# Kernel tuning notes

Measured on AMD Instinct MI355X. Metric: run time of the kernel, lower is better.

## Reference

```python
import jax, jax.numpy as jnp
import numpy as np

HIST_LEN = 100  # STDP history cap in the original module


def setup_inputs() -> dict:
    key = jax.random.key(0)
    ks = jax.random.split(key, 5)
    H, B = 1024, 16384
    return {
        "x": jax.random.normal(ks[0], (B, H), dtype=jnp.float32),
        "weights": jax.random.normal(ks[1], (H, H), dtype=jnp.float32) * 0.1,
        "meta_plasticity": jnp.ones((H,), dtype=jnp.float32),
        "pre_hist": jax.random.normal(ks[2], (HIST_LEN, H), dtype=jnp.float32) * 0.1,
        "post_hist": jax.random.normal(ks[3], (HIST_LEN, H), dtype=jnp.float32) * 0.1,
        "activity_history": jnp.zeros((1000,), dtype=jnp.float32),
        "history_pointer": 5,
        "stdp_window": jnp.float32(20.0),
        "stdp_decay": jnp.float32(0.1),
        "target_activity": jnp.float32(0.1),
        "homeostatic_rate": jnp.float32(0.01),
        "meta_learning_rate": jnp.float32(0.001),
    }


def reference(x, weights, meta_plasticity, pre_hist, post_hist,
              activity_history, history_pointer, stdp_window, stdp_decay,
              target_activity, homeostatic_rate, meta_learning_rate):
    # --- forward matmul: weights * meta_plasticity scales columns (broadcast over rows)
    output = x @ (weights * meta_plasticity)  # [B, H]

    # --- STDP update (vectorized form of the python loop over the history) ---
    # append current mean activities, pop oldest (steady-state length == HIST_LEN)
    pre = jnp.concatenate([pre_hist[1:], x.mean(axis=0)[None]], axis=0)       # [L, H]
    post = jnp.concatenate([post_hist[1:], output.mean(axis=0)[None]], axis=0)
    L = HIST_LEN
    i = jnp.arange(L, dtype=jnp.float32)
    dt = (L - i) * stdp_window
    w = 0.01 * jnp.exp(-dt * stdp_decay)                                      # [L]
    pos_w = jnp.where(i < L - 1, w, 0.0)   # i < len-1 branch
    neg_w = jnp.where(i > 0, w, 0.0)       # i > 0 branch
    # sum_i pos_w[i] * outer(post[-1], pre[i]) = outer(post[-1], pos_w @ pre)
    dW = jnp.outer(post[-1], pos_w @ pre) - jnp.outer(neg_w @ post, pre[-1])
    new_w = jnp.clip(weights + dW, -1.0, 1.0)

    # --- homeostatic plasticity ---
    hist = activity_history.at[history_pointer].set(output.mean())
    activity_diff = target_activity - hist.mean()
    new_w = jnp.clip(new_w * (1.0 + homeostatic_rate * activity_diff), -1.0, 1.0)

    # --- meta plasticity ---
    new_meta = jnp.clip(
        meta_plasticity + meta_learning_rate * (output.mean(axis=0) - meta_plasticity),
        0.0, 2.0)

    return output, new_w, new_meta, hist
```

## Files before the change

kernel.cpp:

```cpp
#include <hip/hip_runtime.h>
#include <hip/hip_bf16.h>

#define H 1024
#define BATCH 16384

typedef unsigned short u16;
typedef u16 u16x8 __attribute__((ext_vector_type(8)));
typedef __bf16 bf16x8 __attribute__((ext_vector_type(8)));
typedef float f32x4 __attribute__((ext_vector_type(4)));

typedef __attribute__((address_space(3))) unsigned int lds_uint;
typedef __attribute__((address_space(1))) const unsigned int glob_uint;

__device__ __forceinline__ u16 f2bf(float f) {
  unsigned int u = __float_as_uint(f);
  u += 0x7fffu + ((u >> 16) & 1u);
  return (u16)(u >> 16);
}

#define WS_XSUMP   0
#define WS_XSUM    (WS_XSUMP + 256 * H)
#define WS_ORAWP   (WS_XSUM + H)
#define WS_POSVP   (WS_ORAWP + 16 * H)
#define WS_NEGHP   (WS_POSVP + 5 * H)
#define WS_SCRATCH (WS_NEGHP + 5 * H)
#define WS_BF16    (WS_SCRATCH + 16)

__global__ __launch_bounds__(256) void prep_kernel(const float* __restrict__ X,
                                                   const float* __restrict__ W,
                                                   u16* __restrict__ Xb,
                                                   u16* __restrict__ Wbt,
                                                   float* __restrict__ ws,
                                                   const float* __restrict__ pre,
                                                   const float* __restrict__ post,
                                                   const float* __restrict__ win,
                                                   const float* __restrict__ dec) {
  __shared__ __align__(16) u16 t[64][72];
  const int b = blockIdx.x, tid = threadIdx.x;
  if (b < 256) {
    size_t r0 = (size_t)b * 64;
    float s0 = 0.f, s1 = 0.f, s2 = 0.f, s3 = 0.f;
#pragma unroll 4
    for (int r = 0; r < 64; ++r) {
      size_t off = (r0 + r) * H + tid * 4;
      const float4 v = *(const float4*)&X[off];
      ushort4 h;
      h.x = f2bf(v.x); h.y = f2bf(v.y); h.z = f2bf(v.z); h.w = f2bf(v.w);
      *(ushort4*)&Xb[off] = h;
      s0 += v.x; s1 += v.y; s2 += v.z; s3 += v.w;
    }
    float* row = &ws[WS_XSUMP + b * H];
    row[tid * 4 + 0] = s0; row[tid * 4 + 1] = s1;
    row[tid * 4 + 2] = s2; row[tid * 4 + 3] = s3;
  } else if (b < 512) {
    const int b2 = b - 256;
    const int n0 = (b2 & 15) * 64, k0 = (b2 >> 4) * 64;
    const int rb = tid >> 4, c4 = tid & 15;
#pragma unroll
    for (int i = 0; i < 4; ++i) {
      int r = rb + i * 16;
      const float4 v = *(const float4*)&W[(size_t)(k0 + r) * H + n0 + c4 * 4];
      t[c4 * 4 + 0][r] = f2bf(v.x);
      t[c4 * 4 + 1][r] = f2bf(v.y);
      t[c4 * 4 + 2][r] = f2bf(v.z);
      t[c4 * 4 + 3][r] = f2bf(v.w);
    }
    __syncthreads();
    const int seg = tid & 7;
#pragma unroll
    for (int p = 0; p < 2; ++p) {
      int wr = p * 32 + (tid >> 3);
      *(u16x8*)&Wbt[(size_t)(n0 + wr) * H + k0 + seg * 8] = *(const u16x8*)&t[wr][seg * 8];
    }
  } else {
    const int b2 = b - 512;
    const int col = (b2 & 3) * 256 + tid;
    const int seg = b2 >> 2;
    const int t0 = 1 + seg * 20;
    int tend = t0 + 20; if (tend > 100) tend = 100;
    float wd = win[0] * dec[0];
    float ps = 0.f, ns = 0.f;
    for (int tt = t0; tt < tend; ++tt) {
      float w = 0.01f * expf(-(float)(101 - tt) * wd);
      ps += w * pre[tt * H + col];
      if (tt >= 2) ns += w * post[tt * H + col];
    }
    ws[WS_POSVP + seg * H + col] = ps;
    ws[WS_NEGHP + seg * H + col] = ns;
  }
}

__global__ __launch_bounds__(512, 2) void gemm_vm_kernel(const u16* __restrict__ Xb,
                                                         const u16* __restrict__ Wbt,
                                                         const float* __restrict__ meta,
                                                         const float* __restrict__ W,
                                                         float* __restrict__ ws,
                                                         float* __restrict__ out) {
  __shared__ __align__(16) u16 lds[65536];

  const int b = blockIdx.x, tid = threadIdx.x;

  if (b >= 256) {
    float* xs = (float*)lds;
    const int b2 = b - 256;
    const int jx = b2 & 3, ky = b2 >> 2;
    if (tid < 64) {
      float s = 0.f;
      const float* p = &ws[WS_XSUMP + ky * 64 + tid];
#pragma unroll 8
      for (int q = 0; q < 256; ++q) s += p[q * H];
      xs[tid] = s;
      if (jx == 0) ws[WS_XSUM + ky * 64 + tid] = s;
    }
    __syncthreads();
    if (tid < 256) {
      const int j = jx * 256 + tid;
      float s = 0.f;
#pragma unroll 8
      for (int k = 0; k < 64; ++k) s += xs[k] * W[(size_t)(ky * 64 + k) * H + j];
      ws[WS_ORAWP + ky * H + j] = s * (1.0f / (float)BATCH);
    }
    return;
  }

  const int tile = ((b & 7) << 5) | (b >> 3);
  const int mt = tile >> 2, nt = tile & 3;
  const size_t row0 = (size_t)mt * 256;
  const int col0 = nt * 256;
  const int wid = tid >> 6, lane = tid & 63;
  const int wm = wid >> 2, wn = wid & 3;
  const int quad = lane >> 4, l16 = lane & 15;
  const int xsw = l16 & 7;

  const int srow = lane >> 3;
  const int schunk = (lane & 7) ^ (srow & 7);

  auto stageA = [&](int t, int h) {
#pragma unroll
    for (int s = 0; s < 2; ++s) {
      const u16* ga = &Xb[(row0 + h * 128 + s * 64 + wid * 8 + srow) * H + t * 64 + schunk * 8];
      lds_uint* ld = (lds_uint*)&lds[(((2 * t + h) & 3) * 8192) + s * 4096 + wid * 512];
      __builtin_amdgcn_global_load_lds((glob_uint*)ga, ld, 16, 0, 0);
    }
  };
  auto stageB = [&](int t, int h) {
#pragma unroll
    for (int s = 0; s < 2; ++s) {
      const u16* gb = &Wbt[(size_t)(col0 + h * 128 + s * 64 + wid * 8 + srow) * H + t * 64 + schunk * 8];
      lds_uint* ld = (lds_uint*)&lds[32768 + (((2 * t + h) & 3) * 8192) + s * 4096 + wid * 512];
      __builtin_amdgcn_global_load_lds((glob_uint*)gb, ld, 16, 0, 0);
    }
  };

  f32x4 acc[8][4];
#pragma unroll
  for (int i = 0; i < 8; ++i)
#pragma unroll
    for (int j = 0; j < 4; ++j) acc[i][j] = (f32x4){0.f, 0.f, 0.f, 0.f};

  stageA(0, 0); stageA(0, 1); stageB(0, 0); stageB(0, 1); stageB(1, 0); stageB(1, 1);
  asm volatile("s_waitcnt vmcnt(2)" ::: "memory");
  __builtin_amdgcn_s_barrier();

  for (int t = 0; t < 16; ++t) {
    const int aslot = ((2 * t + wm) & 3) * 8192;
    const int bslot = 32768 + ((2 * t + (wn >> 1)) & 3) * 8192;
    const int brl = (wn & 1) * 64;
    bf16x8 bv[4][2];

    if (t < 15) { stageA(t + 1, 0); stageA(t + 1, 1); }
#pragma unroll
    for (int fn = 0; fn < 4; ++fn)
#pragma unroll
      for (int ks = 0; ks < 2; ++ks)
        bv[fn][ks] = __builtin_bit_cast(bf16x8,
          *(const u16x8*)&lds[bslot + (brl + fn * 16 + l16) * 64 + (((ks * 4 + quad) ^ xsw) * 8)]);
    {
      bf16x8 av[4][2];
#pragma unroll
      for (int fi = 0; fi < 4; ++fi)
#pragma unroll
        for (int ks = 0; ks < 2; ++ks)
          av[fi][ks] = __builtin_bit_cast(bf16x8,
            *(const u16x8*)&lds[aslot + (fi * 16 + l16) * 64 + (((ks * 4 + quad) ^ xsw) * 8)]);
      asm volatile("s_waitcnt lgkmcnt(0)" ::: "memory");
      __builtin_amdgcn_sched_barrier(0);
      __builtin_amdgcn_s_setprio(1);
#pragma unroll
      for (int fi = 0; fi < 4; ++fi)
#pragma unroll
        for (int fn = 0; fn < 4; ++fn)
#pragma unroll
          for (int ks = 0; ks < 2; ++ks)
            acc[fi][fn] = __builtin_amdgcn_mfma_f32_16x16x32_bf16(
                av[fi][ks], bv[fn][ks], acc[fi][fn], 0, 0, 0);
      __builtin_amdgcn_s_setprio(0);
    }
    __builtin_amdgcn_s_barrier();

    if (t < 14) { stageB(t + 2, 0); stageB(t + 2, 1); }
    {
      bf16x8 av[4][2];
#pragma unroll
      for (int fi = 0; fi < 4; ++fi)
#pragma unroll
        for (int ks = 0; ks < 2; ++ks)
          av[fi][ks] = __builtin_bit_cast(bf16x8,
            *(const u16x8*)&lds[aslot + ((4 + fi) * 16 + l16) * 64 + (((ks * 4 + quad) ^ xsw) * 8)]);
      asm volatile("s_waitcnt lgkmcnt(0)" ::: "memory");
      __builtin_amdgcn_sched_barrier(0);
      __builtin_amdgcn_s_setprio(1);
#pragma unroll
      for (int fi = 0; fi < 4; ++fi)
#pragma unroll
        for (int fn = 0; fn < 4; ++fn)
#pragma unroll
          for (int ks = 0; ks < 2; ++ks)
            acc[4 + fi][fn] = __builtin_amdgcn_mfma_f32_16x16x32_bf16(
                av[fi][ks], bv[fn][ks], acc[4 + fi][fn], 0, 0, 0);
      __builtin_amdgcn_s_setprio(0);
    }
    if (t < 14)       asm volatile("s_waitcnt vmcnt(2)" ::: "memory");
    else if (t == 14) asm volatile("s_waitcnt vmcnt(0)" ::: "memory");
    __builtin_amdgcn_s_barrier();
  }

  float mcol[4];
#pragma unroll
  for (int fn = 0; fn < 4; ++fn) mcol[fn] = meta[col0 + wn * 64 + fn * 16 + l16];
#pragma unroll
  for (int fm = 0; fm < 8; ++fm) {
#pragma unroll
    for (int fn = 0; fn < 4; ++fn) {
      const int col = col0 + wn * 64 + fn * 16 + l16;
#pragma unroll
      for (int r = 0; r < 4; ++r) {
        size_t row = row0 + wm * 128 + fm * 16 + quad * 4 + r;
        out[row * H + col] = acc[fm][fn][r] * mcol[fn];
      }
    }
  }
}

__global__ __launch_bounds__(256) void tail_kernel(const float* __restrict__ W,
                                                   const float* __restrict__ meta,
                                                   const float* __restrict__ act,
                                                   const int* __restrict__ ptr,
                                                   const float* __restrict__ targ,
                                                   const float* __restrict__ homeo,
                                                   const float* __restrict__ mlr,
                                                   const float* __restrict__ win,
                                                   const float* __restrict__ dec,
                                                   const float* __restrict__ ws,
                                                   float* __restrict__ out_w,
                                                   float* __restrict__ meta_out,
                                                   float* __restrict__ hist_out) {
  __shared__ float r1[4], r2[4];
  const int r = blockIdx.x;
  const int t = threadIdx.x;
  const int c4 = t * 4;

  f32x4 oraw = (f32x4){0.f, 0.f, 0.f, 0.f};
#pragma unroll
  for (int i = 0; i < 16; ++i) {
    const float4 v = *(const float4*)&ws[WS_ORAWP + i * H + c4];
    oraw[0] += v.x; oraw[1] += v.y; oraw[2] += v.z; oraw[3] += v.w;
  }
  const float4 mv = *(const float4*)&meta[c4];
  f32x4 om;
  om[0] = mv.x * oraw[0]; om[1] = mv.y * oraw[1];
  om[2] = mv.z * oraw[2]; om[3] = mv.w * oraw[3];

  float s1 = om[0] + om[1] + om[2] + om[3];
  float s2 = 0.f;
#pragma unroll
  for (int j = 0; j < 4; ++j) {
    int idx = t + j * 256;
    if (idx < 1000) s2 += act[idx];
  }
#pragma unroll
  for (int o = 32; o > 0; o >>= 1) {
    s1 += __shfl_down(s1, o, 64);
    s2 += __shfl_down(s2, o, 64);
  }
  if ((t & 63) == 0) { r1[t >> 6] = s1; r2[t >> 6] = s2; }
  __syncthreads();
  const float ts1 = r1[0] + r1[1] + r1[2] + r1[3];
  const float ts2 = r2[0] + r2[1] + r2[2] + r2[3];
  const float total_mean = ts1 / (float)H;
  const int p = ptr[0];
  const float hist_mean = (ts2 - act[p] + total_mean) / 1000.f;
  const float scale = 1.f + homeo[0] * (targ[0] - hist_mean);
  const float w99 = 0.01f * expf(-win[0] * dec[0]);

  float oraw_r = 0.f;
#pragma unroll
  for (int i = 0; i < 16; ++i) oraw_r += ws[WS_ORAWP + i * H + r];
  const float om_r = meta[r] * oraw_r;
  float negh_r = 0.f;
#pragma unroll
  for (int i = 0; i < 5; ++i) negh_r += ws[WS_NEGHP + i * H + r];
  const float neg_r = negh_r + w99 * om_r;

  f32x4 pv = (f32x4){0.f, 0.f, 0.f, 0.f};
#pragma unroll
  for (int i = 0; i < 5; ++i) {
    const float4 v = *(const float4*)&ws[WS_POSVP + i * H + c4];
    pv[0] += v.x; pv[1] += v.y; pv[2] += v.z; pv[3] += v.w;
  }
  const float4 xv = *(const float4*)&ws[WS_XSUM + c4];
  float xx[4] = {xv.x, xv.y, xv.z, xv.w};
  const float4 wv = *(const float4*)&W[(size_t)r * H + c4];
  float wx[4] = {wv.x, wv.y, wv.z, wv.w};
  float4 o;
  float ox[4];
#pragma unroll
  for (int i = 0; i < 4; ++i) {
    float v = wx[i] + om_r * pv[i] - neg_r * (xx[i] * (1.0f / (float)BATCH));
    v = fminf(fmaxf(v, -1.f), 1.f);
    v = v * scale;
    ox[i] = fminf(fmaxf(v, -1.f), 1.f);
  }
  o.x = ox[0]; o.y = ox[1]; o.z = ox[2]; o.w = ox[3];
  *(float4*)&out_w[(size_t)r * H + c4] = o;

  if (r == 0) {
    float4 nm;
    float nx[4] = {mv.x, mv.y, mv.z, mv.w};
    float nr[4];
#pragma unroll
    for (int i = 0; i < 4; ++i) {
      float v = nx[i] + mlr[0] * (om[i] - nx[i]);
      nr[i] = fminf(fmaxf(v, 0.f), 2.f);
    }
    nm.x = nr[0]; nm.y = nr[1]; nm.z = nr[2]; nm.w = nr[3];
    *(float4*)&meta_out[c4] = nm;
#pragma unroll
    for (int j = 0; j < 4; ++j) {
      int idx = t + j * 256;
      if (idx < 1000) hist_out[idx] = (idx == p) ? total_mean : act[idx];
    }
  }
}

__global__ __launch_bounds__(256) void colsum_kernel(const float* __restrict__ x,
                                                     float* __restrict__ xsum) {
  int col = blockIdx.x * 256 + threadIdx.x;
  size_t r0 = (size_t)blockIdx.y * 256;
  float s = 0.f;
#pragma unroll 8
  for (int r = 0; r < 256; ++r) s += x[(r0 + r) * H + col];
  atomicAdd(&xsum[col], s);
}

__global__ __launch_bounds__(256) void gemm_fallback_kernel(const float* __restrict__ X,
                                                            const float* __restrict__ W,
                                                            const float* __restrict__ meta,
                                                            float* __restrict__ out) {
  __shared__ __align__(16) u16 lA[128][40];
  __shared__ __align__(16) u16 lB[128][40];
  const int tid = threadIdx.x;
  const int wave = tid >> 6;
  const int lane = tid & 63;
  const int quad = lane >> 4;
  const int l16 = lane & 15;
  const int wm = wave >> 1, wn = wave & 1;
  const size_t row0 = (size_t)blockIdx.x * 128;
  const int col0 = blockIdx.y * 128;
  f32x4 acc[4][4];
#pragma unroll
  for (int i = 0; i < 4; ++i)
#pragma unroll
    for (int j = 0; j < 4; ++j) acc[i][j] = (f32x4){0.f, 0.f, 0.f, 0.f};
  for (int k0 = 0; k0 < H; k0 += 32) {
#pragma unroll
    for (int i = 0; i < 4; ++i) {
      int idx = i * 256 + tid;
      int r = idx >> 3, c4 = idx & 7;
      const float4 v = *(const float4*)&X[(row0 + r) * H + k0 + c4 * 4];
      ushort4 h;
      h.x = f2bf(v.x); h.y = f2bf(v.y); h.z = f2bf(v.z); h.w = f2bf(v.w);
      *(ushort4*)&lA[r][c4 * 4] = h;
    }
#pragma unroll
    for (int i = 0; i < 4; ++i) {
      int idx = i * 256 + tid;
      int kk = idx >> 5, c4 = idx & 31;
      const float4 v = *(const float4*)&W[(size_t)(k0 + kk) * H + col0 + c4 * 4];
      lB[c4 * 4 + 0][kk] = f2bf(v.x);
      lB[c4 * 4 + 1][kk] = f2bf(v.y);
      lB[c4 * 4 + 2][kk] = f2bf(v.z);
      lB[c4 * 4 + 3][kk] = f2bf(v.w);
    }
    __syncthreads();
    bf16x8 av[4], bv[4];
#pragma unroll
    for (int f = 0; f < 4; ++f) {
      av[f] = __builtin_bit_cast(bf16x8, *(const u16x8*)&lA[wm * 64 + f * 16 + l16][quad * 8]);
      bv[f] = __builtin_bit_cast(bf16x8, *(const u16x8*)&lB[wn * 64 + f * 16 + l16][quad * 8]);
    }
#pragma unroll
    for (int fm = 0; fm < 4; ++fm)
#pragma unroll
      for (int fn = 0; fn < 4; ++fn)
        acc[fm][fn] = __builtin_amdgcn_mfma_f32_16x16x32_bf16(av[fm], bv[fn], acc[fm][fn], 0, 0, 0);
    __syncthreads();
  }
  float mcol[4];
#pragma unroll
  for (int fn = 0; fn < 4; ++fn) mcol[fn] = meta[col0 + wn * 64 + fn * 16 + l16];
#pragma unroll
  for (int fm = 0; fm < 4; ++fm) {
#pragma unroll
    for (int fn = 0; fn < 4; ++fn) {
      int col = col0 + wn * 64 + fn * 16 + l16;
#pragma unroll
      for (int r = 0; r < 4; ++r) {
        size_t row = row0 + wm * 64 + fm * 16 + quad * 4 + r;
        out[row * H + col] = acc[fm][fn][r] * mcol[fn];
      }
    }
  }
}

__global__ __launch_bounds__(256) void vecmat_kernel(const float* __restrict__ W,
                                                     const float* __restrict__ xsum,
                                                     float* __restrict__ outraw) {
  int j = blockIdx.x * 256 + threadIdx.x;
  int k0 = blockIdx.y * 64;
  float s = 0.f;
#pragma unroll 8
  for (int k = 0; k < 64; ++k) s += xsum[k0 + k] * W[(size_t)(k0 + k) * H + j];
  atomicAdd(&outraw[j], s * (1.0f / (float)BATCH));
}

__global__ __launch_bounds__(256) void stdpvec_kernel(const float* __restrict__ pre,
                                                      const float* __restrict__ post,
                                                      const float* __restrict__ win,
                                                      const float* __restrict__ dec,
                                                      float* __restrict__ posv,
                                                      float* __restrict__ negh) {
  int col = blockIdx.x * 256 + threadIdx.x;
  int t0 = 1 + blockIdx.y * 20;
  float wd = win[0] * dec[0];
  float ps = 0.f, ns = 0.f;
  int tend = t0 + 20;
  if (tend > 100) tend = 100;
  for (int t = t0; t < tend; ++t) {
    float w = 0.01f * expf(-(float)(101 - t) * wd);
    ps += w * pre[t * H + col];
    if (t >= 2) ns += w * post[t * H + col];
  }
  atomicAdd(&posv[col], ps);
  atomicAdd(&negh[col], ns);
}

__global__ __launch_bounds__(1024) void finalize_kernel(const float* __restrict__ meta,
                                                        const float* __restrict__ act,
                                                        const int* __restrict__ ptr,
                                                        const float* __restrict__ targ,
                                                        const float* __restrict__ homeo,
                                                        const float* __restrict__ mlr,
                                                        const float* __restrict__ outraw,
                                                        float* __restrict__ outmean,
                                                        float* __restrict__ scalep,
                                                        float* __restrict__ meta_out,
                                                        float* __restrict__ hist_out) {
  __shared__ float r1[16], r2[16];
  __shared__ float sc[2];
  int t = threadIdx.x;
  float om = meta[t] * outraw[t];
  outmean[t] = om;
  float a = (t < 1000) ? act[t] : 0.f;
  float s1 = om, s2 = a;
#pragma unroll
  for (int o = 32; o > 0; o >>= 1) {
    s1 += __shfl_down(s1, o, 64);
    s2 += __shfl_down(s2, o, 64);
  }
  if ((t & 63) == 0) { r1[t >> 6] = s1; r2[t >> 6] = s2; }
  __syncthreads();
  if (t == 0) {
    float ts1 = 0.f, ts2 = 0.f;
#pragma unroll
    for (int i = 0; i < 16; ++i) { ts1 += r1[i]; ts2 += r2[i]; }
    float total_mean = ts1 / (float)H;
    int p = ptr[0];
    float hist_mean = (ts2 - act[p] + total_mean) / 1000.f;
    float diff = targ[0] - hist_mean;
    sc[0] = 1.f + homeo[0] * diff;
    sc[1] = total_mean;
    scalep[0] = sc[0];
  }
  __syncthreads();
  float nm = meta[t] + mlr[0] * (om - meta[t]);
  nm = fminf(fmaxf(nm, 0.f), 2.f);
  meta_out[t] = nm;
  if (t < 1000) hist_out[t] = (t == ptr[0]) ? sc[1] : act[t];
}

__global__ __launch_bounds__(256) void neww_kernel(const float* __restrict__ W,
                                                   const float* __restrict__ outmean,
                                                   const float* __restrict__ posv,
                                                   const float* __restrict__ negh,
                                                   const float* __restrict__ xsum,
                                                   const float* __restrict__ scalep,
                                                   const float* __restrict__ win,
                                                   const float* __restrict__ dec,
                                                   float* __restrict__ out) {
  int idx4 = blockIdx.x * 256 + threadIdx.x;
  int rr = idx4 >> 8;
  int c4 = (idx4 & 255) * 4;
  float w99 = 0.01f * expf(-win[0] * dec[0]);
  float scale = scalep[0];
  float om_r = outmean[rr];
  float neg_r = negh[rr] + w99 * om_r;
  const float4 wv = *(const float4*)&W[(size_t)rr * H + c4];
  const float4 pv = *(const float4*)&posv[c4];
  const float4 xv = *(const float4*)&xsum[c4];
  float4 o;
  float vx[4] = {wv.x, wv.y, wv.z, wv.w};
  float px[4] = {pv.x, pv.y, pv.z, pv.w};
  float xx[4] = {xv.x, xv.y, xv.z, xv.w};
  float ox[4];
#pragma unroll
  for (int i = 0; i < 4; ++i) {
    float v = vx[i] + om_r * px[i] - neg_r * (xx[i] * (1.0f / (float)BATCH));
    v = fminf(fmaxf(v, -1.f), 1.f);
    v = v * scale;
    ox[i] = fminf(fmaxf(v, -1.f), 1.f);
  }
  o.x = ox[0]; o.y = ox[1]; o.z = ox[2]; o.w = ox[3];
  *(float4*)&out[(size_t)rr * H + c4] = o;
}

extern "C" void kernel_launch(void* const* d_in, const int* in_sizes, int n_in,
                              void* d_out, int out_size, void* d_ws, size_t ws_size,
                              hipStream_t stream) {
  const float* x     = (const float*)d_in[0];
  const float* W     = (const float*)d_in[1];
  const float* meta  = (const float*)d_in[2];
  const float* pre   = (const float*)d_in[3];
  const float* post  = (const float*)d_in[4];
  const float* act   = (const float*)d_in[5];
  const int*   ptr   = (const int*)d_in[6];
  const float* win   = (const float*)d_in[7];
  const float* dec   = (const float*)d_in[8];
  const float* targ  = (const float*)d_in[9];
  const float* homeo = (const float*)d_in[10];
  const float* mlr   = (const float*)d_in[11];

  float* out_y    = (float*)d_out;
  float* out_w    = out_y + (size_t)BATCH * H;
  float* out_meta = out_w + (size_t)H * H;
  float* out_hist = out_meta + H;

  float* ws = (float*)d_ws;
  u16* Xb  = (u16*)(ws + WS_BF16);
  u16* Wbt = Xb + (size_t)BATCH * H;

  const size_t ws_need = (size_t)WS_BF16 * sizeof(float) +
                         ((size_t)BATCH * H + (size_t)H * H) * sizeof(u16);

  if (ws_size >= ws_need) {
    prep_kernel<<<532, 256, 0, stream>>>(x, W, Xb, Wbt, ws, pre, post, win, dec);
    gemm_vm_kernel<<<320, 512, 0, stream>>>(Xb, Wbt, meta, W, ws, out_y);
    tail_kernel<<<1024, 256, 0, stream>>>(W, meta, act, ptr, targ, homeo, mlr,
                                          win, dec, ws, out_w, out_meta, out_hist);
  } else {
    float* xsum    = ws;
    float* outraw  = ws + 1024;
    float* outmean = ws + 2048;
    float* posv    = ws + 3072;
    float* negh    = ws + 4096;
    float* scalep  = ws + 5120;
    hipMemsetAsync(d_ws, 0, 6144 * sizeof(float), stream);
    colsum_kernel<<<dim3(4, 64), 256, 0, stream>>>(x, xsum);
    gemm_fallback_kernel<<<dim3(128, 8), 256, 0, stream>>>(x, W, meta, out_y);
    vecmat_kernel<<<dim3(4, 16), 256, 0, stream>>>(W, xsum, outraw);
    stdpvec_kernel<<<dim3(4, 5), 256, 0, stream>>>(pre, post, win, dec, posv, negh);
    finalize_kernel<<<1, 1024, 0, stream>>>(meta, act, ptr, targ, homeo, mlr,
                                            outraw, outmean, scalep, out_meta, out_hist);
    neww_kernel<<<1024, 256, 0, stream>>>(W, outmean, posv, negh, xsum, scalep, win, dec, out_w);
  }
}
```

Before: 203.7 us.

## Fuse prep, GEMM and tail into one cooperative persistent kernel with grid syncs

Replaces the three-kernel sequence (prep, GEMM plus vecmat, tail) with a single cooperative kernel of 256 blocks. It runs the bf16 conversion and transpose, the GEMM, the vec-mat reduction and the weight/meta update as phases separated by grid.sync, and falls back to the old launches if the cooperative launch fails. The goal is to remove launch gaps and tail effects between kernels. In exchange, each phase is limited to 256 blocks, the vecmat phase leaves most blocks idle, and each grid barrier adds its own cost. The vmcnt wait threshold in the pipelined GEMM also changes from 2 to 4, which loosens load synchronization.

```diff
diff --git a/kernel.cpp b/kernel.cpp
--- a/kernel.cpp
+++ b/kernel.cpp
@@ -1,5 +1,8 @@
 #include <hip/hip_runtime.h>
 #include <hip/hip_bf16.h>
+#include <hip/hip_cooperative_groups.h>
+
+namespace cg = cooperative_groups;
 
 #define H 1024
 #define BATCH 16384
@@ -25,6 +28,330 @@
 #define WS_NEGHP   (WS_POSVP + 5 * H)
 #define WS_SCRATCH (WS_NEGHP + 5 * H)
 #define WS_BF16    (WS_SCRATCH + 16)
+
+__global__ __launch_bounds__(512, 2) void fused_kernel(
+    const float* __restrict__ X, const float* __restrict__ W,
+    u16* __restrict__ Xb, u16* __restrict__ Wbt,
+    const float* __restrict__ meta, float* __restrict__ ws,
+    const float* __restrict__ pre, const float* __restrict__ post,
+    const float* __restrict__ act, const int* __restrict__ ptr,
+    const float* __restrict__ win, const float* __restrict__ dec,
+    const float* __restrict__ targ, const float* __restrict__ homeo,
+    const float* __restrict__ mlr,
+    float* __restrict__ out_y, float* __restrict__ out_w,
+    float* __restrict__ out_meta, float* __restrict__ hist_out) {
+  __shared__ __align__(16) u16 lds[65536];
+  const int b = blockIdx.x, tid = threadIdx.x;
+  cg::grid_group grid = cg::this_grid();
+
+  {
+    const int h = tid >> 8;
+    const int c4i = (tid & 255) * 4;
+    const size_t r0 = (size_t)b * 64 + h * 32;
+    float s0 = 0.f, s1 = 0.f, s2 = 0.f, s3 = 0.f;
+#pragma unroll 4
+    for (int r = 0; r < 32; ++r) {
+      size_t off = (r0 + r) * H + c4i;
+      const float4 v = *(const float4*)&X[off];
+      ushort4 hv;
+      hv.x = f2bf(v.x); hv.y = f2bf(v.y); hv.z = f2bf(v.z); hv.w = f2bf(v.w);
+      *(ushort4*)&Xb[off] = hv;
+      s0 += v.x; s1 += v.y; s2 += v.z; s3 += v.w;
+    }
+    float* xpart = (float*)lds;
+    if (h == 1) {
+      xpart[c4i + 0] = s0; xpart[c4i + 1] = s1;
+      xpart[c4i + 2] = s2; xpart[c4i + 3] = s3;
+    }
+    __syncthreads();
+    if (h == 0) {
+      float* row = &ws[WS_XSUMP + b * H];
+      row[c4i + 0] = s0 + xpart[c4i + 0];
+      row[c4i + 1] = s1 + xpart[c4i + 1];
+      row[c4i + 2] = s2 + xpart[c4i + 2];
+      row[c4i + 3] = s3 + xpart[c4i + 3];
+    }
+    __syncthreads();
+  }
+  {
+    u16 (*tt)[72] = (u16 (*)[72])lds;
+    const int n0 = (b & 15) * 64, k0 = (b >> 4) * 64;
+    if (tid < 256) {
+      const int rb = tid >> 4, c4 = tid & 15;
+#pragma unroll
+      for (int i = 0; i < 4; ++i) {
+        int r = rb + i * 16;
+        const float4 v = *(const float4*)&W[(size_t)(k0 + r) * H + n0 + c4 * 4];
+        tt[c4 * 4 + 0][r] = f2bf(v.x);
+        tt[c4 * 4 + 1][r] = f2bf(v.y);
+        tt[c4 * 4 + 2][r] = f2bf(v.z);
+        tt[c4 * 4 + 3][r] = f2bf(v.w);
+      }
+    }
+    __syncthreads();
+    if (tid < 256) {
+      const int seg = tid & 7;
+#pragma unroll
+      for (int p2 = 0; p2 < 2; ++p2) {
+        int wr = p2 * 32 + (tid >> 3);
+        *(u16x8*)&Wbt[(size_t)(n0 + wr) * H + k0 + seg * 8] = *(const u16x8*)&tt[wr][seg * 8];
+      }
+    }
+  }
+  if (b < 20 && tid < 256) {
+    const int col = (b & 3) * 256 + tid;
+    const int seg = b >> 2;
+    const int t0 = 1 + seg * 20;
+    int tend = t0 + 20; if (tend > 100) tend = 100;
+    float wd = win[0] * dec[0];
+    float ps = 0.f, ns = 0.f;
+    for (int ts = t0; ts < tend; ++ts) {
+      float w = 0.01f * expf(-(float)(101 - ts) * wd);
+      ps += w * pre[ts * H + col];
+      if (ts >= 2) ns += w * post[ts * H + col];
+    }
+    ws[WS_POSVP + seg * H + col] = ps;
+    ws[WS_NEGHP + seg * H + col] = ns;
+  }
+  grid.sync();
+
+  {
+    const int tile = ((b & 7) << 5) | (b >> 3);
+    const int mt = tile >> 2, nt = tile & 3;
+    const size_t row0 = (size_t)mt * 256;
+    const int col0 = nt * 256;
+    const int wid = tid >> 6, lane = tid & 63;
+    const int wm = wid >> 2, wn = wid & 3;
+    const int quad = lane >> 4, l16 = lane & 15;
+    const int xsw = l16 & 7;
+
+    const int srow = lane >> 3;
+    const int schunk = (lane & 7) ^ (srow & 7);
+
+    auto stageA = [&](int t, int h) {
+#pragma unroll
+      for (int s = 0; s < 2; ++s) {
+        const u16* ga = &Xb[(row0 + h * 128 + s * 64 + wid * 8 + srow) * H + t * 64 + schunk * 8];
+        lds_uint* ld = (lds_uint*)&lds[(((2 * t + h) & 3) * 8192) + s * 4096 + wid * 512];
+        __builtin_amdgcn_global_load_lds((glob_uint*)ga, ld, 16, 0, 0);
+      }
+    };
+    auto stageB = [&](int t, int h) {
+#pragma unroll
+      for (int s = 0; s < 2; ++s) {
+        const u16* gb = &Wbt[(size_t)(col0 + h * 128 + s * 64 + wid * 8 + srow) * H + t * 64 + schunk * 8];
+        lds_uint* ld = (lds_uint*)&lds[32768 + (((2 * t + h) & 3) * 8192) + s * 4096 + wid * 512];
+        __builtin_amdgcn_global_load_lds((glob_uint*)gb, ld, 16, 0, 0);
+      }
+    };
+
+    f32x4 acc[8][4];
+#pragma unroll
+    for (int i = 0; i < 8; ++i)
+#pragma unroll
+      for (int j = 0; j < 4; ++j) acc[i][j] = (f32x4){0.f, 0.f, 0.f, 0.f};
+
+    stageA(0, 0); stageA(0, 1); stageB(0, 0); stageB(0, 1); stageB(1, 0); stageB(1, 1);
+    asm volatile("s_waitcnt vmcnt(4)" ::: "memory");
+    __builtin_amdgcn_s_barrier();
+
+    for (int t = 0; t < 16; ++t) {
+      const int aslot = ((2 * t + wm) & 3) * 8192;
+      const int bslot = 32768 + ((2 * t + (wn >> 1)) & 3) * 8192;
+      const int brl = (wn & 1) * 64;
+      bf16x8 bv[4][2];
+
+      if (t < 15) { stageA(t + 1, 0); stageA(t + 1, 1); }
+#pragma unroll
+      for (int fn = 0; fn < 4; ++fn)
+#pragma unroll
+        for (int ks = 0; ks < 2; ++ks)
+          bv[fn][ks] = __builtin_bit_cast(bf16x8,
+            *(const u16x8*)&lds[bslot + (brl + fn * 16 + l16) * 64 + (((ks * 4 + quad) ^ xsw) * 8)]);
+      {
+        bf16x8 av[4][2];
+#pragma unroll
+        for (int fi = 0; fi < 4; ++fi)
+#pragma unroll
+          for (int ks = 0; ks < 2; ++ks)
+            av[fi][ks] = __builtin_bit_cast(bf16x8,
+              *(const u16x8*)&lds[aslot + (fi * 16 + l16) * 64 + (((ks * 4 + quad) ^ xsw) * 8)]);
+        asm volatile("s_waitcnt lgkmcnt(0)" ::: "memory");
+        __builtin_amdgcn_sched_barrier(0);
+        __builtin_amdgcn_s_setprio(1);
+#pragma unroll
+        for (int fi = 0; fi < 4; ++fi)
+#pragma unroll
+          for (int fn = 0; fn < 4; ++fn)
+#pragma unroll
+            for (int ks = 0; ks < 2; ++ks)
+              acc[fi][fn] = __builtin_amdgcn_mfma_f32_16x16x32_bf16(
+                  av[fi][ks], bv[fn][ks], acc[fi][fn], 0, 0, 0);
+        __builtin_amdgcn_s_setprio(0);
+      }
+      __builtin_amdgcn_s_barrier();
+
+      if (t < 14) { stageB(t + 2, 0); stageB(t + 2, 1); }
+      {
+        bf16x8 av[4][2];
+#pragma unroll
+        for (int fi = 0; fi < 4; ++fi)
+#pragma unroll
+          for (int ks = 0; ks < 2; ++ks)
+            av[fi][ks] = __builtin_bit_cast(bf16x8,
+              *(const u16x8*)&lds[aslot + ((4 + fi) * 16 + l16) * 64 + (((ks * 4 + quad) ^ xsw) * 8)]);
+        asm volatile("s_waitcnt lgkmcnt(0)" ::: "memory");
+        __builtin_amdgcn_sched_barrier(0);
+        __builtin_amdgcn_s_setprio(1);
+#pragma unroll
+        for (int fi = 0; fi < 4; ++fi)
+#pragma unroll
+          for (int fn = 0; fn < 4; ++fn)
+#pragma unroll
+            for (int ks = 0; ks < 2; ++ks)
+              acc[4 + fi][fn] = __builtin_amdgcn_mfma_f32_16x16x32_bf16(
+                  av[fi][ks], bv[fn][ks], acc[4 + fi][fn], 0, 0, 0);
+        __builtin_amdgcn_s_setprio(0);
+      }
+      if (t < 14)       asm volatile("s_waitcnt vmcnt(4)" ::: "memory");
+      else if (t == 14) asm volatile("s_waitcnt vmcnt(0)" ::: "memory");
+      __builtin_amdgcn_s_barrier();
+    }
+
+    float mcol[4];
+#pragma unroll
+    for (int fn = 0; fn < 4; ++fn) mcol[fn] = meta[col0 + wn * 64 + fn * 16 + l16];
+#pragma unroll
+    for (int fm = 0; fm < 8; ++fm) {
+#pragma unroll
+      for (int fn = 0; fn < 4; ++fn) {
+        const int col = col0 + wn * 64 + fn * 16 + l16;
+#pragma unroll
+        for (int r = 0; r < 4; ++r) {
+          size_t row = row0 + wm * 128 + fm * 16 + quad * 4 + r;
+          out_y[row * H + col] = acc[fm][fn][r] * mcol[fn];
+        }
+      }
+    }
+  }
+  grid.sync();
+
+  if (b < 64) {
+    float* xs = (float*)lds;
+    const int jx = b & 3, ky = b >> 2;
+    if (tid < 64) {
+      float s = 0.f;
+      const float* p = &ws[WS_XSUMP + ky * 64 + tid];
+#pragma unroll 8
+      for (int q = 0; q < 256; ++q) s += p[q * H];
+      xs[tid] = s;
+      if (jx == 0) ws[WS_XSUM + ky * 64 + tid] = s;
+    }
+    __syncthreads();
+    if (tid < 256) {
+      const int j = jx * 256 + tid;
+      float s = 0.f;
+#pragma unroll 8
+      for (int k = 0; k < 64; ++k) s += xs[k] * W[(size_t)(ky * 64 + k) * H + j];
+      ws[WS_ORAWP + ky * H + j] = s * (1.0f / (float)BATCH);
+    }
+  }
+  grid.sync();
+
+  {
+    float* rr1 = (float*)lds;
+    float* rr2 = rr1 + 8;
+    const int c4 = (tid & 255) * 4;
+    f32x4 om = (f32x4){0.f, 0.f, 0.f, 0.f};
+    float4 mv = make_float4(0.f, 0.f, 0.f, 0.f);
+    float s1 = 0.f, s2 = 0.f;
+    if (tid < 256) {
+      f32x4 oraw = (f32x4){0.f, 0.f, 0.f, 0.f};
+#pragma unroll
+      for (int i = 0; i < 16; ++i) {
+        const float4 v = *(const float4*)&ws[WS_ORAWP + i * H + c4];
+        oraw[0] += v.x; oraw[1] += v.y; oraw[2] += v.z; oraw[3] += v.w;
+      }
+      mv = *(const float4*)&meta[c4];
+      om[0] = mv.x * oraw[0]; om[1] = mv.y * oraw[1];
+      om[2] = mv.z * oraw[2]; om[3] = mv.w * oraw[3];
+      s1 = om[0] + om[1] + om[2] + om[3];
+#pragma unroll
+      for (int j = 0; j < 4; ++j) {
+        int idx = tid + j * 256;
+        if (idx < 1000) s2 += act[idx];
+      }
+    }
+#pragma unroll
+    for (int o = 32; o > 0; o >>= 1) {
+      s1 += __shfl_down(s1, o, 64);
+      s2 += __shfl_down(s2, o, 64);
+    }
+    if ((tid & 63) == 0) { rr1[tid >> 6] = s1; rr2[tid >> 6] = s2; }
+    __syncthreads();
+    float ts1 = 0.f, ts2 = 0.f;
+#pragma unroll
+    for (int i = 0; i < 8; ++i) { ts1 += rr1[i]; ts2 += rr2[i]; }
+    const float total_mean = ts1 / (float)H;
+    const int p = ptr[0];
+    const float hist_mean = (ts2 - act[p] + total_mean) / 1000.f;
+    const float scale = 1.f + homeo[0] * (targ[0] - hist_mean);
+    const float w99 = 0.01f * expf(-win[0] * dec[0]);
+
+    if (tid < 256) {
+      f32x4 pv = (f32x4){0.f, 0.f, 0.f, 0.f};
+#pragma unroll
+      for (int i = 0; i < 5; ++i) {
+        const float4 v = *(const float4*)&ws[WS_POSVP + i * H + c4];
+        pv[0] += v.x; pv[1] += v.y; pv[2] += v.z; pv[3] += v.w;
+      }
+      const float4 xv = *(const float4*)&ws[WS_XSUM + c4];
+      const float xx[4] = {xv.x, xv.y, xv.z, xv.w};
+      const float px[4] = {pv[0], pv[1], pv[2], pv[3]};
+#pragma unroll
+      for (int j = 0; j < 4; ++j) {
+        const int r = b * 4 + j;
+        float oraw_r = 0.f;
+#pragma unroll
+        for (int i = 0; i < 16; ++i) oraw_r += ws[WS_ORAWP + i * H + r];
+        const float om_r = meta[r] * oraw_r;
+        float negh_r = 0.f;
+#pragma unroll
+        for (int i = 0; i < 5; ++i) negh_r += ws[WS_NEGHP + i * H + r];
+        const float neg_r = negh_r + w99 * om_r;
+        const float4 wv = *(const float4*)&W[(size_t)r * H + c4];
+        const float wx[4] = {wv.x, wv.y, wv.z, wv.w};
+        float4 o; float ox[4];
+#pragma unroll
+        for (int i = 0; i < 4; ++i) {
+          float v = wx[i] + om_r * px[i] - neg_r * (xx[i] * (1.0f / (float)BATCH));
+          v = fminf(fmaxf(v, -1.f), 1.f);
+          v = v * scale;
+          ox[i] = fminf(fmaxf(v, -1.f), 1.f);
+        }
+        o.x = ox[0]; o.y = ox[1]; o.z = ox[2]; o.w = ox[3];
+        *(float4*)&out_w[(size_t)r * H + c4] = o;
+      }
+      if (b == 0) {
+        float4 nm;
+        const float nx[4] = {mv.x, mv.y, mv.z, mv.w};
+        float nr[4];
+#pragma unroll
+        for (int i = 0; i < 4; ++i) {
+          float v = nx[i] + mlr[0] * (om[i] - nx[i]);
+          nr[i] = fminf(fmaxf(v, 0.f), 2.f);
+        }
+        nm.x = nr[0]; nm.y = nr[1]; nm.z = nr[2]; nm.w = nr[3];
+        *(float4*)&out_meta[c4] = nm;
+#pragma unroll
+        for (int j = 0; j < 4; ++j) {
+          int idx = tid + j * 256;
+          if (idx < 1000) hist_out[idx] = (idx == p) ? total_mean : act[idx];
+        }
+      }
+    }
+  }
+}
 
 __global__ __launch_bounds__(256) void prep_kernel(const float* __restrict__ X,
                                                    const float* __restrict__ W,
@@ -97,7 +424,6 @@
                                                          float* __restrict__ ws,
                                                          float* __restrict__ out) {
   __shared__ __align__(16) u16 lds[65536];
-
   const int b = blockIdx.x, tid = threadIdx.x;
 
   if (b >= 256) {
@@ -131,7 +457,6 @@
   const int wm = wid >> 2, wn = wid & 3;
   const int quad = lane >> 4, l16 = lane & 15;
   const int xsw = l16 & 7;
-
   const int srow = lane >> 3;
   const int schunk = (lane & 7) ^ (srow & 7);
 
@@ -159,7 +484,7 @@
     for (int j = 0; j < 4; ++j) acc[i][j] = (f32x4){0.f, 0.f, 0.f, 0.f};
 
   stageA(0, 0); stageA(0, 1); stageB(0, 0); stageB(0, 1); stageB(1, 0); stageB(1, 1);
-  asm volatile("s_waitcnt vmcnt(2)" ::: "memory");
+  asm volatile("s_waitcnt vmcnt(4)" ::: "memory");
   __builtin_amdgcn_s_barrier();
 
   for (int t = 0; t < 16; ++t) {
@@ -220,7 +545,7 @@
                 av[fi][ks], bv[fn][ks], acc[4 + fi][fn], 0, 0, 0);
       __builtin_amdgcn_s_setprio(0);
     }
-    if (t < 14)       asm volatile("s_waitcnt vmcnt(2)" ::: "memory");
+    if (t < 14)       asm volatile("s_waitcnt vmcnt(4)" ::: "memory");
     else if (t == 14) asm volatile("s_waitcnt vmcnt(0)" ::: "memory");
     __builtin_amdgcn_s_barrier();
   }
@@ -563,10 +888,19 @@
                          ((size_t)BATCH * H + (size_t)H * H) * sizeof(u16);
 
   if (ws_size >= ws_need) {
-    prep_kernel<<<532, 256, 0, stream>>>(x, W, Xb, Wbt, ws, pre, post, win, dec);
-    gemm_vm_kernel<<<320, 512, 0, stream>>>(Xb, Wbt, meta, W, ws, out_y);
-    tail_kernel<<<1024, 256, 0, stream>>>(W, meta, act, ptr, targ, homeo, mlr,
-                                          win, dec, ws, out_w, out_meta, out_hist);
+    void* kargs[] = {
+      (void*)&x, (void*)&W, (void*)&Xb, (void*)&Wbt, (void*)&meta,
+      (void*)&ws, (void*)&pre, (void*)&post, (void*)&act, (void*)&ptr,
+      (void*)&win, (void*)&dec, (void*)&targ, (void*)&homeo, (void*)&mlr,
+      (void*)&out_y, (void*)&out_w, (void*)&out_meta, (void*)&out_hist};
+    hipError_t ce = hipLaunchCooperativeKernel((void*)fused_kernel, dim3(256), dim3(512),
+                                               kargs, 0, stream);
+    if (ce != hipSuccess) {
+      prep_kernel<<<532, 256, 0, stream>>>(x, W, Xb, Wbt, ws, pre, post, win, dec);
+      gemm_vm_kernel<<<320, 512, 0, stream>>>(Xb, Wbt, meta, W, ws, out_y);
+      tail_kernel<<<1024, 256, 0, stream>>>(W, meta, act, ptr, targ, homeo, mlr,
+                                            win, dec, ws, out_w, out_meta, out_hist);
+    }
   } else {
     float* xsum    = ws;
     float* outraw  = ws + 1024;
```

New measurement: 315.4 us. 1.55x slower.
